# Kernel tuning notes

Measured on AMD Instinct MI355X. Metric: run time of the kernel, lower is better.

Reference implementation:

```python
import jax, jax.numpy as jnp
import numpy as np
from math import factorial

N_ATOM = 32768
NODE_DIM = 128
HID = 64
MUL = 16          # hidden multiplicity per irrep
INS = [(0,0,0),(0,2,2),(1,1,0),(1,1,1),(1,1,2),(2,0,2),(2,2,0),(2,2,1),(2,2,2)]  # (l1,l2,l_out)
W_NUMEL = len(INS)*MUL*MUL  # 2304 per-sample tp weights

# ---------- real Clebsch-Gordan coefficients (e3nn-style, Frobenius-normalized) ----------
def _su2_cg(j1,j2,j3,m1,m2,m3):
    if m3 != m1+m2 or not (abs(j1-j2) <= j3 <= j1+j2):
        return 0.0
    f = factorial
    pref = np.sqrt((2*j3+1)*f(j3+j1-j2)*f(j3-j1+j2)*f(j1+j2-j3)/f(j1+j2+j3+1))
    pref *= np.sqrt(f(j3+m3)*f(j3-m3)*f(j1-m1)*f(j1+m1)*f(j2-m2)*f(j2+m2))
    s = 0.0
    for v in range(max(0, j2-j3-m1, j1-j3+m2), min(j1+j2-j3, j1-m1, j2+m2)+1):
        s += (-1)**v/(f(v)*f(j1+j2-j3-v)*f(j1-m1-v)*f(j2+m2-v)*f(j3-j2+m1+v)*f(j3-j1-m2+v))
    return pref*s

def _r2c(l):
    q = np.zeros((2*l+1,2*l+1), dtype=complex)
    for m in range(-l, 0):
        q[l+m, l+abs(m)] = 1/np.sqrt(2); q[l+m, l-abs(m)] = -1j/np.sqrt(2)
    q[l, l] = 1.0
    for m in range(1, l+1):
        q[l+m, l+abs(m)] = (-1)**m/np.sqrt(2); q[l+m, l-abs(m)] = 1j*(-1)**m/np.sqrt(2)
    return (-1j)**l * q

def real_cg(l1, l2, l3):
    C = np.zeros((2*l1+1,2*l2+1,2*l3+1), dtype=complex)
    for m1 in range(-l1, l1+1):
        for m2 in range(-l2, l2+1):
            m3 = m1+m2
            if abs(m3) <= l3:
                C[l1+m1, l2+m2, l3+m3] = _su2_cg(l1,l2,l3,m1,m2,m3)
    Cr = np.einsum('ij,kl,nm,ikn->jlm', _r2c(l1), _r2c(l2), np.conj(_r2c(l3)), C)
    re, im = np.real(Cr), np.imag(Cr)
    out = re if np.linalg.norm(re) >= np.linalg.norm(im) else im
    return (out / np.linalg.norm(out)).astype(np.float32)

_CG = {ins: real_cg(*ins) for ins in set(INS)}
# change of basis: irreps 1x0e+1x1e+1x2e (dim 9) -> cartesian 3x3 rank-2 tensor
_QF = np.concatenate([np.sqrt(2*l+1)*real_cg(l,1,1) for l in range(3)], 0).reshape(9,9).astype(np.float32)
_PERM = np.array([2,0,1])  # e3nn (y,z,x) -> cartesian (x,y,z)


def setup_inputs() -> dict:
    key = jax.random.key(0)
    ks = jax.random.split(key, 12)
    n = lambda k, s: jax.random.normal(k, s, dtype=jnp.float32)
    return {
        "x_scalar": n(ks[0], (N_ATOM, NODE_DIM)),
        "x_spherical": n(ks[1], (N_ATOM, 128 + 64*3 + 32*5)),
        "w_pre0": n(ks[2], (128, MUL)),
        "w_pre1": n(ks[3], (64, MUL)),
        "w_pre2": n(ks[4], (32, MUL)),
        "gw1": n(ks[5], (NODE_DIM, HID)) / float(np.sqrt(NODE_DIM)),
        "gb1": jnp.zeros((HID,), jnp.float32),
        "gw2": n(ks[6], (HID, W_NUMEL)) / float(np.sqrt(HID)),
        "gb2": jnp.zeros((W_NUMEL,), jnp.float32),
        "wpost0": n(ks[7], (3*MUL, 1)),
        "wpost1": n(ks[8], (2*MUL, 1)),
        "wpost2": n(ks[9], (4*MUL, 1)),
    }


def reference(x_scalar, x_spherical, w_pre0, w_pre1, w_pre2, gw1, gb1, gw2, gb2, wpost0, wpost1, wpost2):
    N = x_scalar.shape[0]
    # split edge irreps 128x0e + 64x1o + 32x2e
    x0 = x_spherical[:, :128]
    x1 = x_spherical[:, 128:320].reshape(N, 64, 3)
    x2 = x_spherical[:, 320:].reshape(N, 32, 5)
    # pre o3.Linear (per-l channel mixing, fan-in normalized)
    h = [
        (x0 @ w_pre0)[:, :, None] / float(np.sqrt(128.0)),              # [N,16,1] 0e
        jnp.einsum('num,uv->nvm', x1, w_pre1) / float(np.sqrt(64.0)),    # [N,16,3] 1o
        jnp.einsum('num,uv->nvm', x2, w_pre2) / float(np.sqrt(32.0)),    # [N,16,5] 2e
    ]
    # gate MLP -> per-sample tp weights [N, n_ins, u, w]
    g = (jax.nn.silu(x_scalar @ gw1 + gb1) @ gw2 + gb2).reshape(N, len(INS), MUL, MUL)
    # 'uuw' CG tensor product
    outs = {0: [], 1: [], 2: []}
    inv_sqrt_mul = float(1.0 / np.sqrt(MUL))
    for idx, (i, j, lo) in enumerate(INS):
        C = jnp.asarray(_CG[(i, j, lo)])
        o = jnp.einsum('nuw,abm,nua,nub->nwm', g[:, idx], C, h[i], h[j]) * inv_sqrt_mul
        outs[lo].append(o)
    # post o3.Linear: (48x0e + 32x1e + 64x2e) -> 1x0e + 1x1e + 1x2e
    wpost = [wpost0, wpost1, wpost2]
    ys = []
    for lo in range(3):
        z = jnp.concatenate(outs[lo], axis=1)                       # [N, n_paths*MUL, 2lo+1]
        y = jnp.einsum('num,uv->nvm', z, wpost[lo]) / float(np.sqrt(z.shape[1]))
        ys.append(y.reshape(N, 2*lo+1))
    atom_out = jnp.concatenate(ys, axis=1)                           # [N,9]
    # change of basis to cartesian rank-2 tensor + axis reindexing
    res = (atom_out @ jnp.asarray(_QF)).reshape(N, 3, 3)
    return res[:, _PERM][:, :, _PERM]
```

## Files before the change

kernel.cpp:

```cpp
#include <hip/hip_runtime.h>

#define NA 32768

typedef float  f32x4  __attribute__((ext_vector_type(4)));
typedef __bf16 bf16x8 __attribute__((ext_vector_type(8)));
typedef unsigned short u16x8 __attribute__((ext_vector_type(8)));
typedef unsigned short u16x4 __attribute__((ext_vector_type(4)));


__device__ __forceinline__ unsigned short bf16u(float f) {
    unsigned int x = __float_as_uint(f);
    x += 0x7FFFu + ((x >> 16) & 1u);
    return (unsigned short)(x >> 16);
}
__device__ __forceinline__ unsigned short cvt1(float f) {
    return __builtin_bit_cast(unsigned short, (__bf16)f);
}
__device__ __forceinline__ f32x4 MFMA16(u16x8 a, u16x8 b, f32x4 c) {
    return __builtin_amdgcn_mfma_f32_16x16x32_bf16(
        __builtin_bit_cast(bf16x8, a), __builtin_bit_cast(bf16x8, b), c, 0, 0, 0);
}

__global__ void setup_kernel(const float* __restrict__ gw1,
                             const float* __restrict__ gw2, const float* __restrict__ gb2,
                             const float* __restrict__ w_pre0, const float* __restrict__ w_pre1,
                             const float* __restrict__ w_pre2,
                             const float* __restrict__ wpost0, const float* __restrict__ wpost1,
                             const float* __restrict__ wpost2,
                             unsigned short* __restrict__ wsS, float* __restrict__ b2p)
{
    const int t = blockIdx.x * 256 + threadIdx.x;
    const int LO[9]  = {0,2,0,1,2,2,0,1,2};
    const int POS[9] = {0,0,1,0,1,2,2,1,3};
    const float SCALE[3] = {0.036084391824351615f,
                            0.04419417382415922f,
                            0.03125f};
    if (t < 8192) {
        const int j = t & 7, lane = (t >> 3) & 63, kt = (t >> 9) & 3, ct = t >> 11;
        const int k = kt * 32 + ((lane >> 4) & 3) * 8 + j;
        const int n = ct * 16 + (lane & 15);
        wsS[t] = bf16u(gw1[k * 64 + n]);
    } else if (t < 17408) {
        const int q = t - 8192;
        const int j = q & 7, lane = (q >> 3) & 63, kt = (q >> 9) & 1, ct = q >> 10;
        const int k = kt * 32 + ((lane >> 4) & 3) * 8 + j;
        const int idx = ct, u = lane & 15;
        const int lo = LO[idx];
        const float* wp = (lo == 0) ? wpost0 : (lo == 1) ? wpost1 : wpost2;
        const float* wv = wp + POS[idx] * 16;
        const float* gsrc = gw2 + (size_t)k * 2304 + idx * 256 + u * 16;
        float s = 0.f;
        for (int w = 0; w < 16; ++w) s = fmaf(gsrc[w], wv[w], s);
        wsS[8192 + q] = bf16u(s * SCALE[lo]);
    } else if (t < 19456) {
        const int q = t - 17408;
        const int j = q & 7, lane = (q >> 3) & 63, kt = q >> 9;
        const int k = kt * 32 + ((lane >> 4) & 3) * 8 + j;
        wsS[17408 + q] = bf16u(w_pre0[k * 16 + (lane & 15)] * 0.08838834764831845f);
    } else if (t < 20480) {
        const int q = t - 19456;
        const int j = q & 7, lane = (q >> 3) & 63, kt = q >> 9;
        const int k = kt * 32 + ((lane >> 4) & 3) * 8 + j;
        wsS[19456 + q] = bf16u(w_pre1[k * 16 + (lane & 15)] * 0.125f);
    } else if (t < 20992) {
        const int q = t - 20480;
        const int j = q & 7, lane = (q >> 3) & 63;
        const int k = ((lane >> 4) & 3) * 8 + j;
        wsS[20480 + q] = bf16u(w_pre2[k * 16 + (lane & 15)] * 0.17677669529663687f);
    } else if (t < 21136) {
        const int e = t - 20992;
        const int idx = e >> 4, u = e & 15;
        const int lo = LO[idx];
        const float* wp = (lo == 0) ? wpost0 : (lo == 1) ? wpost1 : wpost2;
        const float* wv = wp + POS[idx] * 16;
        const float* bsrc = gb2 + idx * 256 + u * 16;
        float sb = 0.f;
        for (int w = 0; w < 16; ++w) sb = fmaf(bsrc[w], wv[w], sb);
        b2p[e] = sb * SCALE[lo];
    }
}

#define RR 200
#define SHO 3200

__global__ __launch_bounds__(256, 4) void csc_kernel(
    const float* __restrict__ x_scalar, const float* __restrict__ x_sph,
    const float* __restrict__ gb1,
    const unsigned short* __restrict__ wsS, const float* __restrict__ b2p,
    float* __restrict__ out)
{
    __shared__ __align__(16) unsigned short buf[4][4352];

    const int lane = threadIdx.x & 63;
    const int wvi  = threadIdx.x >> 6;
    const int lm = lane & 15, lg = lane >> 4;
    const int n0 = (blockIdx.x * 4 + wvi) * 16;
    unsigned short* __restrict__ B = buf[wvi];

    const float* __restrict__ srcq = x_sph + (size_t)n0 * 480;

    {
        float4 v[8];
#pragma unroll
        for (int i = 0; i < 8; ++i) {
            const int idx4 = i * 64 + lane;
            const int row = idx4 >> 5, col4 = idx4 & 31;
            v[i] = *(const float4*)(srcq + (size_t)row * 480 + col4 * 4);
        }
#pragma unroll
        for (int i = 0; i < 8; ++i) {
            const int idx4 = i * 64 + lane;
            const int row = idx4 >> 5, col4 = idx4 & 31;
            const u16x4 w = { cvt1(v[i].x), cvt1(v[i].y), cvt1(v[i].z), cvt1(v[i].w) };
            *(u16x4*)&B[row * RR + col4 * 4] = w;
        }
    }
    f32x4 acc0 = (f32x4){0.f,0.f,0.f,0.f};
#pragma unroll
    for (int kt = 0; kt < 4; ++kt) {
        const u16x8 f = *(const u16x8*)&B[lm * RR + kt * 32 + lg * 8];
        acc0 = MFMA16(f, *(const u16x8*)(wsS + 17408 + (size_t)(kt*64+lane)*8), acc0);
    }

    {
        float4 v[12];
#pragma unroll
        for (int i = 0; i < 12; ++i) {
            const int idx4 = i * 64 + lane;
            const int row = idx4 / 48, col4 = idx4 - row * 48;
            v[i] = *(const float4*)(srcq + (size_t)row * 480 + 128 + col4 * 4);
        }
#pragma unroll
        for (int i = 0; i < 12; ++i) {
            const int idx4 = i * 64 + lane;
            const int row = idx4 / 48, col4 = idx4 - row * 48;
            const u16x4 w = { cvt1(v[i].x), cvt1(v[i].y), cvt1(v[i].z), cvt1(v[i].w) };
            *(u16x4*)&B[row * RR + col4 * 4] = w;
        }
    }
    f32x4 accP[3];
    {
        u16x8 f1[3][2];
#pragma unroll
        for (int kt = 0; kt < 2; ++kt) {
            const int base = lm * RR + 96 * kt + 24 * lg;
            const u16x8 sA = *(const u16x8*)&B[base];
            const u16x8 sB = *(const u16x8*)&B[base + 8];
            const u16x8 sC = *(const u16x8*)&B[base + 16];
            unsigned short span[24];
#pragma unroll
            for (int e = 0; e < 8; ++e) { span[e] = sA[e]; span[8+e] = sB[e]; span[16+e] = sC[e]; }
#pragma unroll
            for (int m = 0; m < 3; ++m) {
                u16x8 f;
#pragma unroll
                for (int j = 0; j < 8; ++j) f[j] = span[3 * j + m];
                f1[m][kt] = f;
            }
        }
#pragma unroll
        for (int m = 0; m < 3; ++m) {
            f32x4 acc = (f32x4){0.f,0.f,0.f,0.f};
#pragma unroll
            for (int kt = 0; kt < 2; ++kt)
                acc = MFMA16(f1[m][kt], *(const u16x8*)(wsS + 19456 + (size_t)(kt*64+lane)*8), acc);
            accP[m] = acc;
        }
    }

    {
        float4 v[10];
#pragma unroll
        for (int i = 0; i < 10; ++i) {
            const int idx4 = i * 64 + lane;
            const int row = idx4 / 40, col4 = idx4 - row * 40;
            v[i] = *(const float4*)(srcq + (size_t)row * 480 + 320 + col4 * 4);
        }
#pragma unroll
        for (int i = 0; i < 10; ++i) {
            const int idx4 = i * 64 + lane;
            const int row = idx4 / 40, col4 = idx4 - row * 40;
            const u16x4 w = { cvt1(v[i].x), cvt1(v[i].y), cvt1(v[i].z), cvt1(v[i].w) };
            *(u16x4*)&B[row * RR + col4 * 4] = w;
        }
    }
    f32x4 accQ[5];
    {
        unsigned short span[40];
        const int base = lm * RR + 40 * lg;
#pragma unroll
        for (int c = 0; c < 5; ++c) {
            const u16x8 s = *(const u16x8*)&B[base + c * 8];
#pragma unroll
            for (int e = 0; e < 8; ++e) span[c * 8 + e] = s[e];
        }
#pragma unroll
        for (int m = 0; m < 5; ++m) {
            u16x8 f;
#pragma unroll
            for (int j = 0; j < 8; ++j) f[j] = span[5 * j + m];
            accQ[m] = MFMA16(f, *(const u16x8*)(wsS + 20480 + (size_t)lane*8),
                             (f32x4){0.f,0.f,0.f,0.f});
        }
    }

    {
        const float* __restrict__ src = x_scalar + (size_t)n0 * 128;
        float4 v[8];
#pragma unroll
        for (int i = 0; i < 8; ++i) {
            const int idx4 = i * 64 + lane;
            v[i] = *(const float4*)(src + (size_t)idx4 * 4);
        }
#pragma unroll
        for (int i = 0; i < 8; ++i) {
            const int idx4 = i * 64 + lane;
            const int row = idx4 >> 5, col4 = idx4 & 31;
            const u16x4 w = { cvt1(v[i].x), cvt1(v[i].y), cvt1(v[i].z), cvt1(v[i].w) };
            *(u16x4*)&B[row * RR + col4 * 4] = w;
        }
    }

    f32x4 accA0, accA1, accA2, accA3;
    {
        const float b0 = gb1[lm], b1 = gb1[16 + lm], bv2 = gb1[32 + lm], b3 = gb1[48 + lm];
        accA0 = (f32x4){b0,b0,b0,b0}; accA1 = (f32x4){b1,b1,b1,b1};
        accA2 = (f32x4){bv2,bv2,bv2,bv2}; accA3 = (f32x4){b3,b3,b3,b3};
    }
#pragma unroll
    for (int kt = 0; kt < 4; ++kt) {
        const u16x8 af = *(const u16x8*)&B[lm * RR + kt * 32 + lg * 8];
        accA0 = MFMA16(af, *(const u16x8*)(wsS + (size_t)((0*4+kt)*64+lane)*8), accA0);
        accA1 = MFMA16(af, *(const u16x8*)(wsS + (size_t)((1*4+kt)*64+lane)*8), accA1);
        accA2 = MFMA16(af, *(const u16x8*)(wsS + (size_t)((2*4+kt)*64+lane)*8), accA2);
        accA3 = MFMA16(af, *(const u16x8*)(wsS + (size_t)((3*4+kt)*64+lane)*8), accA3);
    }
#pragma unroll
    for (int r = 0; r < 4; ++r) {
        const int atom = lg * 4 + r;
        const float v0 = accA0[r], v1 = accA1[r], v2 = accA2[r], v3 = accA3[r];
        B[SHO + atom * 72 +  0 + lm] = cvt1(v0 / (1.f + __expf(-v0)));
        B[SHO + atom * 72 + 16 + lm] = cvt1(v1 / (1.f + __expf(-v1)));
        B[SHO + atom * 72 + 32 + lm] = cvt1(v2 / (1.f + __expf(-v2)));
        B[SHO + atom * 72 + 48 + lm] = cvt1(v3 / (1.f + __expf(-v3)));
    }

    const u16x8 hf0 = *(const u16x8*)&B[SHO + lm * 72 + lg * 8];
    const u16x8 hf1 = *(const u16x8*)&B[SHO + lm * 72 + 32 + lg * 8];
    f32x4 gB0, gB1, gB2, gB4, gB5, gB6, gB8;
#define INITB(ACC, CT) { const float b = b2p[(CT)*16 + lm]; ACC = (f32x4){b,b,b,b}; }
    INITB(gB0,0) INITB(gB1,1) INITB(gB2,2) INITB(gB4,4) INITB(gB5,5) INITB(gB6,6) INITB(gB8,8)
#define DOB(ACC, CT) \
    ACC = MFMA16(hf0, *(const u16x8*)(wsS + 8192 + (size_t)(((CT)*2+0)*64+lane)*8), ACC); \
    ACC = MFMA16(hf1, *(const u16x8*)(wsS + 8192 + (size_t)(((CT)*2+1)*64+lane)*8), ACC);
    DOB(gB0,0) DOB(gB1,1) DOB(gB2,2) DOB(gB4,4) DOB(gB5,5) DOB(gB6,6) DOB(gB8,8)

    const float C110 = 0.5773502691896258f;
    const float C220 = 0.4472135954999579f;
    const float Ca = 0.31622776601683794f, Cb = 0.18257418583505536f;
    const float A2 = 0.2390457218668787f, B2c = 0.20701966780270626f, D2 = 0.11952286093343936f;
    const float is3 = 0.5773502691896258f, is6 = 0.4082482904638631f, is2 = 0.7071067811865476f;

#pragma unroll
    for (int r = 0; r < 4; ++r) {
        const int row = lg * 4 + r;
        const float h0 = acc0[r];
        const float p0 = accP[0][r], p1 = accP[1][r], p2 = accP[2][r];
        const float q0 = accQ[0][r], q1 = accQ[1][r], q2 = accQ[2][r],
                    q3 = accQ[3][r], q4 = accQ[4][r];
        const float G0 = gB0[r], G1 = gB1[r], G2 = gB2[r], G4 = gB4[r],
                    G5 = gB5[r], G6 = gB6[r], G8 = gB8[r];

        float y0 = G0 * h0 * h0
                 + G2 * C110 * (p0*p0 + p1*p1 + p2*p2)
                 + G6 * C220 * (q0*q0 + q1*q1 + q2*q2 + q3*q3 + q4*q4);
        float z0, z1, z2, z3, z4;
        {
            const float c15 = C220 * h0 * (G1 + G5);
            z0 = c15 * q0; z1 = c15 * q1; z2 = c15 * q2; z3 = c15 * q3; z4 = c15 * q4;
        }
        z0 = fmaf(G4, 2.f*Ca*p0*p2, z0);
        z1 = fmaf(G4, 2.f*Ca*p0*p1, z1);
        z2 = fmaf(G4, Cb*(2.f*p1*p1 - p0*p0 - p2*p2), z2);
        z3 = fmaf(G4, 2.f*Ca*p2*p1, z3);
        z4 = fmaf(G4, Ca*(p2*p2 - p0*p0), z4);
        z0 = fmaf(G8, -2.f*A2*q0*q2 + 2.f*B2c*q1*q3, z0);
        z1 = fmaf(G8,  2.f*B2c*(q0*q3 - q4*q1) + 2.f*D2*q1*q2, z1);
        z2 = fmaf(G8,  A2*(q2*q2 - q0*q0 - q4*q4) + D2*(q1*q1 + q3*q3), z2);
        z3 = fmaf(G8,  2.f*B2c*(q0*q1 + q3*q4) + 2.f*D2*q2*q3, z3);
        z4 = fmaf(G8, -2.f*A2*q2*q4 + B2c*(q3*q3 - q1*q1), z4);

#pragma unroll
        for (int msk = 1; msk <= 8; msk <<= 1) {
            y0 += __shfl_xor(y0, msk, 64);
            z0 += __shfl_xor(z0, msk, 64);
            z1 += __shfl_xor(z1, msk, 64);
            z2 += __shfl_xor(z2, msk, 64);
            z3 += __shfl_xor(z3, msk, 64);
            z4 += __shfl_xor(z4, msk, 64);
        }

        const float c0 = y0*is3 - z2*is6 - z4*is2;
        const float c4 = y0*is3 + 2.f*z2*is6;
        const float c8 = y0*is3 - z2*is6 + z4*is2;
        const float c1 = z1*is2, c2v = z0*is2, c5 = z3*is2;
        if (lm < 9) {
            const float val = (lm==0)?c8 : (lm==1)?c2v : (lm==2)?c5 : (lm==3)?c2v
                            : (lm==4)?c0 : (lm==5)?c1 : (lm==6)?c5 : (lm==7)?c1 : c4;
            out[(size_t)(n0 + row) * 9 + lm] = val;
        }
    }
}

extern "C" void kernel_launch(void* const* d_in, const int* in_sizes, int n_in,
                              void* d_out, int out_size, void* d_ws, size_t ws_size,
                              hipStream_t stream) {
    const float* x_scalar = (const float*)d_in[0];
    const float* x_sph    = (const float*)d_in[1];
    const float* w_pre0   = (const float*)d_in[2];
    const float* w_pre1   = (const float*)d_in[3];
    const float* w_pre2   = (const float*)d_in[4];
    const float* gw1      = (const float*)d_in[5];
    const float* gb1      = (const float*)d_in[6];
    const float* gw2      = (const float*)d_in[7];
    const float* gb2      = (const float*)d_in[8];
    const float* wpost0   = (const float*)d_in[9];
    const float* wpost1   = (const float*)d_in[10];
    const float* wpost2   = (const float*)d_in[11];

    unsigned short* wsS = (unsigned short*)d_ws;
    float* b2p = (float*)((char*)d_ws + 41984);

    setup_kernel<<<83, 256, 0, stream>>>(gw1, gw2, gb2, w_pre0, w_pre1, w_pre2,
                                         wpost0, wpost1, wpost2, wsS, b2p);
    csc_kernel<<<NA / 64, 256, 0, stream>>>(x_scalar, x_sph, gb1, wsS, b2p, (float*)d_out);
}
```

Before: 27.14 us.

## Stage gate weight tables in shared memory and prefetch projection weights to registers

Each block now cooperatively copies the first 17408 bf16 weight entries (the gate MLP layer-1 and layer-2 fragments) into LDS once and synchronizes, so the MFMA B-operands come from LDS instead of per-wave global loads. Pre-projection weight fragments and biases are hoisted into registers at kernel start, and the per-wave staging buffer shrinks (row stride 168). The l=1 input is staged in two halves to fit the smaller buffer. This cuts redundant global/L2 traffic for weights, at the cost of about 56KB of LDS per block, which limits occupancy, plus a block-wide barrier and more live registers; the launch-bounds occupancy hint is dropped.

```diff
diff --git a/kernel.cpp b/kernel.cpp
--- a/kernel.cpp
+++ b/kernel.cpp
@@ -1,6 +1,8 @@
 #include <hip/hip_runtime.h>
 
 #define NA 32768
+#define RR 168
+#define TAB 17408
 
 typedef float  f32x4  __attribute__((ext_vector_type(4)));
 typedef __bf16 bf16x8 __attribute__((ext_vector_type(8)));
@@ -80,22 +82,52 @@
     }
 }
 
-#define RR 200
-#define SHO 3200
-
-__global__ __launch_bounds__(256, 4) void csc_kernel(
+__global__ __launch_bounds__(256) void csc_kernel(
     const float* __restrict__ x_scalar, const float* __restrict__ x_sph,
     const float* __restrict__ gb1,
     const unsigned short* __restrict__ wsS, const float* __restrict__ b2p,
     float* __restrict__ out)
 {
-    __shared__ __align__(16) unsigned short buf[4][4352];
-
-    const int lane = threadIdx.x & 63;
-    const int wvi  = threadIdx.x >> 6;
+    __shared__ __align__(16) unsigned short all[TAB + 4 * 16 * RR];
+
+    const int tid  = threadIdx.x;
+    const int lane = tid & 63;
+    const int wvi  = tid >> 6;
     const int lm = lane & 15, lg = lane >> 4;
     const int n0 = (blockIdx.x * 4 + wvi) * 16;
-    unsigned short* __restrict__ B = buf[wvi];
+    unsigned short* __restrict__ sTab = all;
+    unsigned short* __restrict__ Bw   = all + TAB + wvi * 16 * RR;
+
+    {
+        u16x8 t[9];
+#pragma unroll
+        for (int i = 0; i < 9; ++i) {
+            const int off = i * 256 + tid;
+            t[i] = (off < 2176) ? *(const u16x8*)(wsS + (size_t)off * 8)
+                                : (u16x8){0,0,0,0,0,0,0,0};
+        }
+#pragma unroll
+        for (int i = 0; i < 9; ++i) {
+            const int off = i * 256 + tid;
+            if (off < 2176) *(u16x8*)&sTab[(size_t)off * 8] = t[i];
+        }
+    }
+
+    u16x8 w0f[4], w1f[2], w2f;
+#pragma unroll
+    for (int kt = 0; kt < 4; ++kt) w0f[kt] = *(const u16x8*)(wsS + 17408 + (size_t)(kt*64+lane)*8);
+#pragma unroll
+    for (int kt = 0; kt < 2; ++kt) w1f[kt] = *(const u16x8*)(wsS + 19456 + (size_t)(kt*64+lane)*8);
+    w2f = *(const u16x8*)(wsS + 20480 + (size_t)lane*8);
+    float bini[7];
+    {
+        const int CTs[7] = {0,1,2,4,5,6,8};
+#pragma unroll
+        for (int c = 0; c < 7; ++c) bini[c] = b2p[CTs[c]*16 + lm];
+    }
+    const float gb0 = gb1[lm], gbq1 = gb1[16+lm], gbq2 = gb1[32+lm], gbq3 = gb1[48+lm];
+
+    __syncthreads();
 
     const float* __restrict__ srcq = x_sph + (size_t)n0 * 480;
 
@@ -104,68 +136,62 @@
 #pragma unroll
         for (int i = 0; i < 8; ++i) {
             const int idx4 = i * 64 + lane;
-            const int row = idx4 >> 5, col4 = idx4 & 31;
-            v[i] = *(const float4*)(srcq + (size_t)row * 480 + col4 * 4);
+            v[i] = *(const float4*)(srcq + (size_t)(idx4 >> 5) * 480 + (idx4 & 31) * 4);
         }
 #pragma unroll
         for (int i = 0; i < 8; ++i) {
             const int idx4 = i * 64 + lane;
-            const int row = idx4 >> 5, col4 = idx4 & 31;
+            const int row = idx4 >> 5, c4 = idx4 & 31;
             const u16x4 w = { cvt1(v[i].x), cvt1(v[i].y), cvt1(v[i].z), cvt1(v[i].w) };
-            *(u16x4*)&B[row * RR + col4 * 4] = w;
+            *(u16x4*)&Bw[row * RR + c4 * 4] = w;
         }
     }
     f32x4 acc0 = (f32x4){0.f,0.f,0.f,0.f};
 #pragma unroll
     for (int kt = 0; kt < 4; ++kt) {
-        const u16x8 f = *(const u16x8*)&B[lm * RR + kt * 32 + lg * 8];
-        acc0 = MFMA16(f, *(const u16x8*)(wsS + 17408 + (size_t)(kt*64+lane)*8), acc0);
-    }
-
-    {
-        float4 v[12];
-#pragma unroll
-        for (int i = 0; i < 12; ++i) {
-            const int idx4 = i * 64 + lane;
-            const int row = idx4 / 48, col4 = idx4 - row * 48;
-            v[i] = *(const float4*)(srcq + (size_t)row * 480 + 128 + col4 * 4);
-        }
-#pragma unroll
-        for (int i = 0; i < 12; ++i) {
-            const int idx4 = i * 64 + lane;
-            const int row = idx4 / 48, col4 = idx4 - row * 48;
+        const u16x8 f = *(const u16x8*)&Bw[lm * RR + kt * 32 + lg * 8];
+        acc0 = MFMA16(f, w0f[kt], acc0);
+    }
+
+    u16x8 f1[3][2];
+#pragma unroll
+    for (int sub = 0; sub < 2; ++sub) {
+        float4 v[6];
+#pragma unroll
+        for (int i = 0; i < 6; ++i) {
+            const int idx4 = i * 64 + lane;
+            const int row = idx4 / 24, c4 = idx4 - row * 24;
+            v[i] = *(const float4*)(srcq + (size_t)row * 480 + 128 + sub * 96 + c4 * 4);
+        }
+#pragma unroll
+        for (int i = 0; i < 6; ++i) {
+            const int idx4 = i * 64 + lane;
+            const int row = idx4 / 24, c4 = idx4 - row * 24;
             const u16x4 w = { cvt1(v[i].x), cvt1(v[i].y), cvt1(v[i].z), cvt1(v[i].w) };
-            *(u16x4*)&B[row * RR + col4 * 4] = w;
+            *(u16x4*)&Bw[row * RR + c4 * 4] = w;
+        }
+        const int base = lm * RR + 24 * lg;
+        const u16x8 sA = *(const u16x8*)&Bw[base];
+        const u16x8 sB = *(const u16x8*)&Bw[base + 8];
+        const u16x8 sC = *(const u16x8*)&Bw[base + 16];
+        unsigned short span[24];
+#pragma unroll
+        for (int e = 0; e < 8; ++e) { span[e] = sA[e]; span[8+e] = sB[e]; span[16+e] = sC[e]; }
+#pragma unroll
+        for (int m = 0; m < 3; ++m) {
+            u16x8 f;
+#pragma unroll
+            for (int j = 0; j < 8; ++j) f[j] = span[3 * j + m];
+            f1[m][sub] = f;
         }
     }
     f32x4 accP[3];
-    {
-        u16x8 f1[3][2];
-#pragma unroll
-        for (int kt = 0; kt < 2; ++kt) {
-            const int base = lm * RR + 96 * kt + 24 * lg;
-            const u16x8 sA = *(const u16x8*)&B[base];
-            const u16x8 sB = *(const u16x8*)&B[base + 8];
-            const u16x8 sC = *(const u16x8*)&B[base + 16];
-            unsigned short span[24];
-#pragma unroll
-            for (int e = 0; e < 8; ++e) { span[e] = sA[e]; span[8+e] = sB[e]; span[16+e] = sC[e]; }
-#pragma unroll
-            for (int m = 0; m < 3; ++m) {
-                u16x8 f;
-#pragma unroll
-                for (int j = 0; j < 8; ++j) f[j] = span[3 * j + m];
-                f1[m][kt] = f;
-            }
-        }
-#pragma unroll
-        for (int m = 0; m < 3; ++m) {
-            f32x4 acc = (f32x4){0.f,0.f,0.f,0.f};
-#pragma unroll
-            for (int kt = 0; kt < 2; ++kt)
-                acc = MFMA16(f1[m][kt], *(const u16x8*)(wsS + 19456 + (size_t)(kt*64+lane)*8), acc);
-            accP[m] = acc;
-        }
+#pragma unroll
+    for (int m = 0; m < 3; ++m) {
+        f32x4 a = (f32x4){0.f,0.f,0.f,0.f};
+        a = MFMA16(f1[m][0], w1f[0], a);
+        a = MFMA16(f1[m][1], w1f[1], a);
+        accP[m] = a;
     }
 
     {
@@ -173,15 +199,15 @@
 #pragma unroll
         for (int i = 0; i < 10; ++i) {
             const int idx4 = i * 64 + lane;
-            const int row = idx4 / 40, col4 = idx4 - row * 40;
-            v[i] = *(const float4*)(srcq + (size_t)row * 480 + 320 + col4 * 4);
+            const int row = idx4 / 40, c4 = idx4 - row * 40;
+            v[i] = *(const float4*)(srcq + (size_t)row * 480 + 320 + c4 * 4);
         }
 #pragma unroll
         for (int i = 0; i < 10; ++i) {
             const int idx4 = i * 64 + lane;
-            const int row = idx4 / 40, col4 = idx4 - row * 40;
+            const int row = idx4 / 40, c4 = idx4 - row * 40;
             const u16x4 w = { cvt1(v[i].x), cvt1(v[i].y), cvt1(v[i].z), cvt1(v[i].w) };
-            *(u16x4*)&B[row * RR + col4 * 4] = w;
+            *(u16x4*)&Bw[row * RR + c4 * 4] = w;
         }
     }
     f32x4 accQ[5];
@@ -190,7 +216,7 @@
         const int base = lm * RR + 40 * lg;
 #pragma unroll
         for (int c = 0; c < 5; ++c) {
-            const u16x8 s = *(const u16x8*)&B[base + c * 8];
+            const u16x8 s = *(const u16x8*)&Bw[base + c * 8];
 #pragma unroll
             for (int e = 0; e < 8; ++e) span[c * 8 + e] = s[e];
         }
@@ -199,8 +225,7 @@
             u16x8 f;
 #pragma unroll
             for (int j = 0; j < 8; ++j) f[j] = span[5 * j + m];
-            accQ[m] = MFMA16(f, *(const u16x8*)(wsS + 20480 + (size_t)lane*8),
-                             (f32x4){0.f,0.f,0.f,0.f});
+            accQ[m] = MFMA16(f, w2f, (f32x4){0.f,0.f,0.f,0.f});
         }
     }
 
@@ -208,51 +233,52 @@
         const float* __restrict__ src = x_scalar + (size_t)n0 * 128;
         float4 v[8];
 #pragma unroll
+        for (int i = 0; i < 8; ++i) v[i] = *(const float4*)(src + (size_t)(i * 64 + lane) * 4);
+#pragma unroll
         for (int i = 0; i < 8; ++i) {
             const int idx4 = i * 64 + lane;
-            v[i] = *(const float4*)(src + (size_t)idx4 * 4);
-        }
-#pragma unroll
-        for (int i = 0; i < 8; ++i) {
-            const int idx4 = i * 64 + lane;
-            const int row = idx4 >> 5, col4 = idx4 & 31;
+            const int row = idx4 >> 5, c4 = idx4 & 31;
             const u16x4 w = { cvt1(v[i].x), cvt1(v[i].y), cvt1(v[i].z), cvt1(v[i].w) };
-            *(u16x4*)&B[row * RR + col4 * 4] = w;
-        }
-    }
-
-    f32x4 accA0, accA1, accA2, accA3;
-    {
-        const float b0 = gb1[lm], b1 = gb1[16 + lm], bv2 = gb1[32 + lm], b3 = gb1[48 + lm];
-        accA0 = (f32x4){b0,b0,b0,b0}; accA1 = (f32x4){b1,b1,b1,b1};
-        accA2 = (f32x4){bv2,bv2,bv2,bv2}; accA3 = (f32x4){b3,b3,b3,b3};
-    }
+            *(u16x4*)&Bw[row * RR + c4 * 4] = w;
+        }
+    }
+    f32x4 accA0 = (f32x4){gb0,gb0,gb0,gb0};
+    f32x4 accA1 = (f32x4){gbq1,gbq1,gbq1,gbq1};
+    f32x4 accA2 = (f32x4){gbq2,gbq2,gbq2,gbq2};
+    f32x4 accA3 = (f32x4){gbq3,gbq3,gbq3,gbq3};
+    u16x8 af[4];
+#pragma unroll
+    for (int kt = 0; kt < 4; ++kt) af[kt] = *(const u16x8*)&Bw[lm * RR + kt * 32 + lg * 8];
 #pragma unroll
     for (int kt = 0; kt < 4; ++kt) {
-        const u16x8 af = *(const u16x8*)&B[lm * RR + kt * 32 + lg * 8];
-        accA0 = MFMA16(af, *(const u16x8*)(wsS + (size_t)((0*4+kt)*64+lane)*8), accA0);
-        accA1 = MFMA16(af, *(const u16x8*)(wsS + (size_t)((1*4+kt)*64+lane)*8), accA1);
-        accA2 = MFMA16(af, *(const u16x8*)(wsS + (size_t)((2*4+kt)*64+lane)*8), accA2);
-        accA3 = MFMA16(af, *(const u16x8*)(wsS + (size_t)((3*4+kt)*64+lane)*8), accA3);
+        accA0 = MFMA16(af[kt], *(const u16x8*)&sTab[(size_t)((0*4+kt)*64+lane)*8], accA0);
+        accA1 = MFMA16(af[kt], *(const u16x8*)&sTab[(size_t)((1*4+kt)*64+lane)*8], accA1);
+        accA2 = MFMA16(af[kt], *(const u16x8*)&sTab[(size_t)((2*4+kt)*64+lane)*8], accA2);
+        accA3 = MFMA16(af[kt], *(const u16x8*)&sTab[(size_t)((3*4+kt)*64+lane)*8], accA3);
     }
 #pragma unroll
     for (int r = 0; r < 4; ++r) {
         const int atom = lg * 4 + r;
         const float v0 = accA0[r], v1 = accA1[r], v2 = accA2[r], v3 = accA3[r];
-        B[SHO + atom * 72 +  0 + lm] = cvt1(v0 / (1.f + __expf(-v0)));
-        B[SHO + atom * 72 + 16 + lm] = cvt1(v1 / (1.f + __expf(-v1)));
-        B[SHO + atom * 72 + 32 + lm] = cvt1(v2 / (1.f + __expf(-v2)));
-        B[SHO + atom * 72 + 48 + lm] = cvt1(v3 / (1.f + __expf(-v3)));
-    }
-
-    const u16x8 hf0 = *(const u16x8*)&B[SHO + lm * 72 + lg * 8];
-    const u16x8 hf1 = *(const u16x8*)&B[SHO + lm * 72 + 32 + lg * 8];
+        Bw[atom * RR +  0 + lm] = cvt1(v0 / (1.f + __expf(-v0)));
+        Bw[atom * RR + 16 + lm] = cvt1(v1 / (1.f + __expf(-v1)));
+        Bw[atom * RR + 32 + lm] = cvt1(v2 / (1.f + __expf(-v2)));
+        Bw[atom * RR + 48 + lm] = cvt1(v3 / (1.f + __expf(-v3)));
+    }
+
+    const u16x8 hf0 = *(const u16x8*)&Bw[lm * RR + lg * 8];
+    const u16x8 hf1 = *(const u16x8*)&Bw[lm * RR + 32 + lg * 8];
     f32x4 gB0, gB1, gB2, gB4, gB5, gB6, gB8;
-#define INITB(ACC, CT) { const float b = b2p[(CT)*16 + lm]; ACC = (f32x4){b,b,b,b}; }
-    INITB(gB0,0) INITB(gB1,1) INITB(gB2,2) INITB(gB4,4) INITB(gB5,5) INITB(gB6,6) INITB(gB8,8)
+    gB0 = (f32x4){bini[0],bini[0],bini[0],bini[0]};
+    gB1 = (f32x4){bini[1],bini[1],bini[1],bini[1]};
+    gB2 = (f32x4){bini[2],bini[2],bini[2],bini[2]};
+    gB4 = (f32x4){bini[3],bini[3],bini[3],bini[3]};
+    gB5 = (f32x4){bini[4],bini[4],bini[4],bini[4]};
+    gB6 = (f32x4){bini[5],bini[5],bini[5],bini[5]};
+    gB8 = (f32x4){bini[6],bini[6],bini[6],bini[6]};
 #define DOB(ACC, CT) \
-    ACC = MFMA16(hf0, *(const u16x8*)(wsS + 8192 + (size_t)(((CT)*2+0)*64+lane)*8), ACC); \
-    ACC = MFMA16(hf1, *(const u16x8*)(wsS + 8192 + (size_t)(((CT)*2+1)*64+lane)*8), ACC);
+    ACC = MFMA16(hf0, *(const u16x8*)&sTab[8192 + (size_t)(((CT)*2+0)*64+lane)*8], ACC); \
+    ACC = MFMA16(hf1, *(const u16x8*)&sTab[8192 + (size_t)(((CT)*2+1)*64+lane)*8], ACC);
     DOB(gB0,0) DOB(gB1,1) DOB(gB2,2) DOB(gB4,4) DOB(gB5,5) DOB(gB6,6) DOB(gB8,8)
 
     const float C110 = 0.5773502691896258f;
```

Measured after the change: 28.03 us. +3.3%, slower.
